# Optimization experiments

Hardware: AMD Instinct MI355X
Metric: run time of the kernel (lower is better)

Reference implementation:

```python
import jax, jax.numpy as jnp
import numpy as np

B, S, D, N = 8, 4096, 1024, 64
SHIFT_FRAC = 0.5
LN_EPS = 1e-5


def setup_inputs() -> dict:
    key = jax.random.key(0)
    ks = jax.random.split(key, 6)
    x = jax.random.normal(ks[0], (B, S, D), jnp.float32)
    # decay in (-1, 0] so w = exp(decay) in (e^-1, 1] -- stable recurrence
    time_decay = -jax.random.uniform(ks[1], (N,), jnp.float32)
    time_first = 0.1 * jax.random.normal(ks[2], (N,), jnp.float32)
    key_w = jax.random.normal(ks[3], (N, D), jnp.float32) / np.float32(np.sqrt(D))
    value_w = jax.random.normal(ks[4], (N, D), jnp.float32) / np.float32(np.sqrt(D))
    output_w = jax.random.normal(ks[5], (D, N), jnp.float32) / np.float32(np.sqrt(N))
    time_shift_gates = jnp.ones((D,), jnp.float32)
    ln_w = jnp.ones((D,), jnp.float32)
    ln_b = jnp.zeros((D,), jnp.float32)
    return dict(x=x, time_decay=time_decay, time_first=time_first,
                key_w=key_w, value_w=value_w, output_w=output_w,
                time_shift_gates=time_shift_gates, ln_w=ln_w, ln_b=ln_b)


def reference(x, time_decay, time_first, key_w, value_w, output_w,
              time_shift_gates, ln_w, ln_b):
    b, s, d = x.shape
    # ---- token shift (blend current token with shifted sequence) ----
    shift = max(1, int(s * SHIFT_FRAC))
    x_cat = jnp.concatenate([x[:, shift:, :], x[:, :-shift, :]], axis=1)  # (b,s,d)
    g = jax.nn.sigmoid(time_shift_gates)
    x_shift = x_cat * g + x * (1.0 - g)
    # ---- LayerNorm (biased variance, eps=1e-5, affine) ----
    mu = jnp.mean(x_shift, axis=-1, keepdims=True)
    var = jnp.mean((x_shift - mu) ** 2, axis=-1, keepdims=True)
    x_norm = (x_shift - mu) * jax.lax.rsqrt(var + LN_EPS) * ln_w + ln_b
    # ---- K/V projections, batched over all timesteps ----
    k = jnp.einsum('bsd,nd->bsn', x_norm, key_w)   # (b,s,N)
    v = jnp.einsum('bsd,nd->bsn', x_norm, value_w)  # (b,s,N)
    w = jnp.exp(time_decay)                          # (N,)
    wkv = jnp.exp(-jnp.exp(time_first) * k) * v      # (b,s,N)
    # ---- sequential linear recurrence: states = states*w + wkv_t ----
    def step(states, wkv_t):
        states = states * w + wkv_t
        return states, states
    init = jnp.zeros((b, wkv.shape[-1]), x.dtype)
    last_states, states_seq = jax.lax.scan(step, init, jnp.swapaxes(wkv, 0, 1))  # (s,b,N)
    # ---- output projection batched outside the loop ----
    output = jnp.einsum('sbn,dn->bsd', states_seq, output_w)  # (b,s,d)
    # dropout is identity in eval mode
    return output, last_states
```

## Files before the change

kernel.cpp:

```cpp
#include <hip/hip_runtime.h>
#include <math.h>

#define B_ 8
#define S_ 4096
#define D_ 1024
#define N_ 64
#define SHIFT_ 2048
#define LCH 32
#define CCH 128
#define MTOT (B_*S_)
#define EPS_ 1e-5f

typedef __attribute__((ext_vector_type(8))) short v8s;
typedef __attribute__((ext_vector_type(4))) float v4f;

static __device__ __forceinline__ short f2bf(float f) {
    unsigned int u = __float_as_uint(f);
    u += 0x7fffu + ((u >> 16) & 1u);
    return (short)(u >> 16);
}

__global__ __launch_bounds__(256) void k_conv(
    const float* __restrict__ keyw, const float* __restrict__ valw,
    const float* __restrict__ ow, const float* __restrict__ tf,
    const float* __restrict__ tsg,
    short* __restrict__ wbf, short* __restrict__ owbf,
    float* __restrict__ etf, float* __restrict__ g) {
    int i = blockIdx.x * 256 + threadIdx.x;
    if (i < 65536)          wbf[i] = f2bf(keyw[i]);
    else if (i < 131072)    wbf[i] = f2bf(valw[i - 65536]);
    else if (i < 196608)    owbf[i - 131072] = f2bf(ow[i - 131072]);
    else if (i < 196672)    etf[i - 196608] = __expf(tf[i - 196608]);
    else if (i < 197696) {
        int j = i - 196672;
        g[j] = 1.0f / (1.0f + __expf(-tsg[j]));
    }
}

__global__ __launch_bounds__(256) void k_stats_fused(
    const float* __restrict__ x, const float* __restrict__ g,
    const float* __restrict__ lnw, const float* __restrict__ lnb,
    short* __restrict__ xn) {
    int b = blockIdx.x >> 11;
    int t = blockIdx.x & 2047;
    const float* rowa = x + ((size_t)(b * S_ + t)) * D_;
    const float* rowb = rowa + (size_t)SHIFT_ * D_;
    int c = threadIdx.x * 4;
    float4 xa = *(const float4*)(rowa + c);
    float4 xb = *(const float4*)(rowb + c);
    float4 gg = *(const float4*)(g + c);
    float av[4] = {xa.x, xa.y, xa.z, xa.w};
    float bv[4] = {xb.x, xb.y, xb.z, xb.w};
    float gv[4] = {gg.x, gg.y, gg.z, gg.w};
    float u[4], w2[4];
    float s1 = 0.f, q1 = 0.f, s2 = 0.f, q2 = 0.f;
#pragma unroll
    for (int j = 0; j < 4; j++) {
        u[j]  = gv[j] * bv[j] + (1.f - gv[j]) * av[j];
        w2[j] = gv[j] * av[j] + (1.f - gv[j]) * bv[j];
        s1 += u[j];  q1 += u[j] * u[j];
        s2 += w2[j]; q2 += w2[j] * w2[j];
    }
    __shared__ float red[4][4];
    int lane = threadIdx.x & 63, wv = threadIdx.x >> 6;
#pragma unroll
    for (int off = 32; off > 0; off >>= 1) {
        s1 += __shfl_down(s1, off);
        q1 += __shfl_down(q1, off);
        s2 += __shfl_down(s2, off);
        q2 += __shfl_down(q2, off);
    }
    if (lane == 0) { red[wv][0] = s1; red[wv][1] = q1; red[wv][2] = s2; red[wv][3] = q2; }
    __syncthreads();
    float S1 = red[0][0] + red[1][0] + red[2][0] + red[3][0];
    float Q1 = red[0][1] + red[1][1] + red[2][1] + red[3][1];
    float S2 = red[0][2] + red[1][2] + red[2][2] + red[3][2];
    float Q2 = red[0][3] + red[1][3] + red[2][3] + red[3][3];
    float m1 = S1 * (1.f / D_), m2 = S2 * (1.f / D_);
    float rs1 = rsqrtf(Q1 * (1.f / D_) - m1 * m1 + EPS_);
    float rs2 = rsqrtf(Q2 * (1.f / D_) - m2 * m2 + EPS_);
    float4 lw = *(const float4*)(lnw + c);
    float4 lb = *(const float4*)(lnb + c);
    float lwv[4] = {lw.x, lw.y, lw.z, lw.w};
    float lbv[4] = {lb.x, lb.y, lb.z, lb.w};
    short o1[4], o2[4];
#pragma unroll
    for (int j = 0; j < 4; j++) {
        o1[j] = f2bf((u[j]  - m1) * rs1 * lwv[j] + lbv[j]);
        o2[j] = f2bf((w2[j] - m2) * rs2 * lwv[j] + lbv[j]);
    }
    short* d1 = xn + ((size_t)(b * S_ + t)) * D_ + c;
    short* d2 = d1 + (size_t)SHIFT_ * D_;
    *(short4*)d1 = make_short4(o1[0], o1[1], o1[2], o1[3]);
    *(short4*)d2 = make_short4(o2[0], o2[1], o2[2], o2[3]);
}

__global__ __launch_bounds__(512) void k_proj_mx(
    const short* __restrict__ xn, const short* __restrict__ wbf,
    const float* __restrict__ etf, const float* __restrict__ tdec,
    float* __restrict__ wkv, float* __restrict__ Acar) {
    __shared__ float C[64 * 132];
    int tid = threadIdx.x, wid = tid >> 6, lane = tid & 63;
    int wm = wid >> 1, wn = wid & 1;
    int quad = lane >> 4, l15 = lane & 15;
    int m0 = blockIdx.x * 64;
    const short* ab = xn + ((size_t)(m0 + wm * 16 + l15)) * D_ + quad * 8;
    const short* bb = wbf + ((size_t)(wn * 64 + l15)) * D_ + quad * 8;
    v4f acc[4];
#pragma unroll
    for (int j = 0; j < 4; j++) acc[j] = (v4f)0.f;

#pragma unroll 4
    for (int k0 = 0; k0 < D_; k0 += 32) {
        v8s a0 = *(const v8s*)(ab + k0);
        v8s b0 = *(const v8s*)(bb + k0);
        v8s b1 = *(const v8s*)(bb + (size_t)16 * D_ + k0);
        v8s b2 = *(const v8s*)(bb + (size_t)32 * D_ + k0);
        v8s b3 = *(const v8s*)(bb + (size_t)48 * D_ + k0);
        acc[0] = __builtin_amdgcn_mfma_f32_16x16x32_bf16(a0, b0, acc[0], 0, 0, 0);
        acc[1] = __builtin_amdgcn_mfma_f32_16x16x32_bf16(a0, b1, acc[1], 0, 0, 0);
        acc[2] = __builtin_amdgcn_mfma_f32_16x16x32_bf16(a0, b2, acc[2], 0, 0, 0);
        acc[3] = __builtin_amdgcn_mfma_f32_16x16x32_bf16(a0, b3, acc[3], 0, 0, 0);
    }
#pragma unroll
    for (int j = 0; j < 4; j++)
#pragma unroll
        for (int r = 0; r < 4; r++)
            C[(wm * 16 + quad * 4 + r) * 132 + wn * 64 + j * 16 + l15] = acc[j][r];
    __syncthreads();

    int tok = tid >> 3, n0 = (tid & 7) * 8;
    float* orow = wkv + ((size_t)(m0 + tok)) * N_ + n0;
    float os[8];
#pragma unroll
    for (int jj = 0; jj < 8; jj++) {
        float kv = C[tok * 132 + n0 + jj];
        float vv = C[tok * 132 + 64 + n0 + jj];
        os[jj] = __expf(-etf[n0 + jj] * kv) * vv;
    }
    *(float4*)(orow + 0) = make_float4(os[0], os[1], os[2], os[3]);
    *(float4*)(orow + 4) = make_float4(os[4], os[5], os[6], os[7]);
#pragma unroll
    for (int jj = 0; jj < 8; jj++) C[tok * 132 + n0 + jj] = os[jj];
    __syncthreads();

    if (tid < 128) {
        int c = tid >> 6, n = tid & 63;
        float w = expf(tdec[n]);
        float s = 0.f;
#pragma unroll
        for (int i = 0; i < LCH; i++) s = s * w + C[(c * 32 + i) * 132 + n];
        Acar[((size_t)blockIdx.x * 2 + c) * N_ + n] = s;
    }
}

__global__ __launch_bounds__(256) void k_stats_mu(const float* __restrict__ x,
                                                  const float* __restrict__ g,
                                                  float* __restrict__ mu,
                                                  float* __restrict__ rstd) {
    int b = blockIdx.x >> 11;
    int t = blockIdx.x & 2047;
    const float* rowa = x + ((size_t)(b * S_ + t)) * D_;
    const float* rowb = rowa + (size_t)SHIFT_ * D_;
    int c = threadIdx.x * 4;
    float4 xa = *(const float4*)(rowa + c);
    float4 xb = *(const float4*)(rowb + c);
    float4 gg = *(const float4*)(g + c);
    float av[4] = {xa.x, xa.y, xa.z, xa.w};
    float bv[4] = {xb.x, xb.y, xb.z, xb.w};
    float gv[4] = {gg.x, gg.y, gg.z, gg.w};
    float s1 = 0.f, q1 = 0.f, s2 = 0.f, q2 = 0.f;
#pragma unroll
    for (int j = 0; j < 4; j++) {
        float u  = gv[j] * bv[j] + (1.f - gv[j]) * av[j];
        float w2 = gv[j] * av[j] + (1.f - gv[j]) * bv[j];
        s1 += u;  q1 += u * u;
        s2 += w2; q2 += w2 * w2;
    }
    __shared__ float red[4][4];
    int lane = threadIdx.x & 63, wv = threadIdx.x >> 6;
#pragma unroll
    for (int off = 32; off > 0; off >>= 1) {
        s1 += __shfl_down(s1, off);
        q1 += __shfl_down(q1, off);
        s2 += __shfl_down(s2, off);
        q2 += __shfl_down(q2, off);
    }
    if (lane == 0) { red[wv][0] = s1; red[wv][1] = q1; red[wv][2] = s2; red[wv][3] = q2; }
    __syncthreads();
    if (threadIdx.x == 0) {
        float S1 = 0, Q1 = 0, S2 = 0, Q2 = 0;
#pragma unroll
        for (int i = 0; i < 4; i++) { S1 += red[i][0]; Q1 += red[i][1]; S2 += red[i][2]; Q2 += red[i][3]; }
        float m1 = S1 * (1.f / D_), m2 = S2 * (1.f / D_);
        float v1 = Q1 * (1.f / D_) - m1 * m1;
        float v2 = Q2 * (1.f / D_) - m2 * m2;
        int m = b * S_ + t;
        mu[m] = m1;           rstd[m] = rsqrtf(v1 + EPS_);
        mu[m + SHIFT_] = m2;  rstd[m + SHIFT_] = rsqrtf(v2 + EPS_);
    }
}

__global__ __launch_bounds__(256) void k_proj_fp32(
    const float* __restrict__ x, const float* __restrict__ keyw,
    const float* __restrict__ valw, const float* __restrict__ g,
    const float* __restrict__ lnw, const float* __restrict__ lnb,
    const float* __restrict__ tf, const float* __restrict__ mu,
    const float* __restrict__ rstd, float* __restrict__ wkv) {
    __shared__ float smem[64 * 132];
    float* As = smem;
    float* Bs = smem + 64 * 36;

    int m0 = blockIdx.x * 64;
    int b = m0 >> 12;
    int t0 = m0 & 4095;
    int t2 = (t0 + SHIFT_) & 4095;
    const float* xa_base = x + ((size_t)(b * S_ + t0)) * D_;
    const float* xb_base = x + ((size_t)(b * S_ + t2)) * D_;

    int tid = threadIdx.x;
    int ty = tid >> 4, tx = tid & 15;
    int tokA = tid >> 3;
    int cA = (tid & 7) * 4;

    float mu0 = mu[m0 + tokA],      rs0 = rstd[m0 + tokA];
    float mu1 = mu[m0 + tokA + 32], rs1 = rstd[m0 + tokA + 32];

    int nB = tid >> 1;
    int halfB = tid & 1;
    const float* wrow = (nB < 64) ? (keyw + (size_t)nB * D_)
                                  : (valw + (size_t)(nB - 64) * D_);

    float acc[4][8];
#pragma unroll
    for (int i = 0; i < 4; i++)
#pragma unroll
        for (int j = 0; j < 8; j++) acc[i][j] = 0.f;

    for (int kk0 = 0; kk0 < D_; kk0 += 32) {
        float4 gg = *(const float4*)(g + kk0 + cA);
        float4 lw = *(const float4*)(lnw + kk0 + cA);
        float4 lb = *(const float4*)(lnb + kk0 + cA);
        float gv[4] = {gg.x, gg.y, gg.z, gg.w};
        float lwv[4] = {lw.x, lw.y, lw.z, lw.w};
        float lbv[4] = {lb.x, lb.y, lb.z, lb.w};
#pragma unroll
        for (int r = 0; r < 2; r++) {
            int tok = tokA + r * 32;
            float4 xa = *(const float4*)(xa_base + (size_t)tok * D_ + kk0 + cA);
            float4 xb = *(const float4*)(xb_base + (size_t)tok * D_ + kk0 + cA);
            float xav[4] = {xa.x, xa.y, xa.z, xa.w};
            float xbv[4] = {xb.x, xb.y, xb.z, xb.w};
            float m_ = r ? mu1 : mu0;
            float rs_ = r ? rs1 : rs0;
#pragma unroll
            for (int j = 0; j < 4; j++) {
                float xs = gv[j] * xbv[j] + (1.f - gv[j]) * xav[j];
                As[tok * 36 + cA + j] = (xs - m_) * rs_ * lwv[j] + lbv[j];
            }
        }
#pragma unroll
        for (int cc = 0; cc < 16; cc += 4) {
            int kk = halfB * 16 + cc;
            float4 wv4 = *(const float4*)(wrow + kk0 + kk);
            Bs[(kk + 0) * 132 + nB] = wv4.x;
            Bs[(kk + 1) * 132 + nB] = wv4.y;
            Bs[(kk + 2) * 132 + nB] = wv4.z;
            Bs[(kk + 3) * 132 + nB] = wv4.w;
        }
        __syncthreads();
#pragma unroll
        for (int kk = 0; kk < 32; kk++) {
            float a0 = As[(ty * 4 + 0) * 36 + kk];
            float a1 = As[(ty * 4 + 1) * 36 + kk];
            float a2 = As[(ty * 4 + 2) * 36 + kk];
            float a3 = As[(ty * 4 + 3) * 36 + kk];
            float bvv[8];
#pragma unroll
            for (int j = 0; j < 8; j++) bvv[j] = Bs[kk * 132 + tx * 8 + j];
#pragma unroll
            for (int j = 0; j < 8; j++) {
                acc[0][j] = fmaf(a0, bvv[j], acc[0][j]);
                acc[1][j] = fmaf(a1, bvv[j], acc[1][j]);
                acc[2][j] = fmaf(a2, bvv[j], acc[2][j]);
                acc[3][j] = fmaf(a3, bvv[j], acc[3][j]);
            }
        }
        __syncthreads();
    }
#pragma unroll
    for (int i = 0; i < 4; i++)
#pragma unroll
        for (int j = 0; j < 8; j++)
            smem[(ty * 4 + i) * 132 + tx * 8 + j] = acc[i][j];
    __syncthreads();
    {
        int tok = tid >> 2;
        int n0 = (tid & 3) * 16;
        float* orow = wkv + ((size_t)(m0 + tok)) * N_ + n0;
#pragma unroll
        for (int jj = 0; jj < 16; jj++) {
            int n = n0 + jj;
            float kv = smem[tok * 132 + n];
            float vv = smem[tok * 132 + 64 + n];
            orow[jj] = __expf(-__expf(tf[n]) * kv) * vv;
        }
    }
}

__global__ __launch_bounds__(64) void k_chunk(const float* __restrict__ wkv,
                                              const float* __restrict__ tdec,
                                              float* __restrict__ Acar) {
    int idx = blockIdx.x;
    int n = threadIdx.x;
    float w = expf(tdec[n]);
    const float* p = wkv + (size_t)idx * (LCH * N_) + n;
    float s = 0.f;
#pragma unroll
    for (int i = 0; i < LCH; i++) s = s * w + p[i * N_];
    Acar[idx * N_ + n] = s;
}

__global__ __launch_bounds__(64) void k_carry(const float* __restrict__ Acar,
                                              const float* __restrict__ tdec,
                                              float* __restrict__ Cin,
                                              float* __restrict__ last) {
    int b = blockIdx.x;
    int n = threadIdx.x;
    float wL = expf(tdec[n] * (float)LCH);
    float c = 0.f;
#pragma unroll 16
    for (int ch = 0; ch < CCH; ch++) {
        Cin[(b * CCH + ch) * N_ + n] = c;
        c = c * wL + Acar[(b * CCH + ch) * N_ + n];
    }
    last[b * N_ + n] = c;
}

__global__ __launch_bounds__(64) void k_rescan(const float* __restrict__ wkv,
                                               const float* __restrict__ Cin,
                                               const float* __restrict__ tdec,
                                               short* __restrict__ st) {
    int idx = blockIdx.x;
    int n = threadIdx.x;
    float w = expf(tdec[n]);
    float s = Cin[idx * N_ + n];
    const float* p = wkv + (size_t)idx * (LCH * N_) + n;
    short* q = st + (size_t)idx * (LCH * N_) + n;
#pragma unroll
    for (int i = 0; i < LCH; i++) { s = s * w + p[i * N_]; q[i * N_] = f2bf(s); }
}

__global__ __launch_bounds__(256) void k_out_mx(const short* __restrict__ st,
                                                const short* __restrict__ owbf,
                                                float* __restrict__ out) {
    __shared__ float C[64 * 132];
    int tid = threadIdx.x, wid = tid >> 6, lane = tid & 63;
    int wm = wid >> 1, wn = wid & 1;
    int quad = lane >> 4, l15 = lane & 15;
    int m0 = (blockIdx.x >> 3) * 64;
    int d0 = (blockIdx.x & 7) * 128;
    const short* ab = st + ((size_t)(m0 + wm * 32 + l15)) * N_ + quad * 8;
    const short* bb = owbf + ((size_t)(d0 + wn * 64 + l15)) * N_ + quad * 8;
    v4f acc[2][4];
#pragma unroll
    for (int i = 0; i < 2; i++)
#pragma unroll
        for (int j = 0; j < 4; j++) acc[i][j] = (v4f)0.f;
#pragma unroll
    for (int ks = 0; ks < 2; ks++) {
        v8s a0 = *(const v8s*)(ab + ks * 32);
        v8s a1 = *(const v8s*)(ab + 16 * N_ + ks * 32);
        v8s b0 = *(const v8s*)(bb + ks * 32);
        v8s b1 = *(const v8s*)(bb + 16 * N_ + ks * 32);
        v8s b2 = *(const v8s*)(bb + 32 * N_ + ks * 32);
        v8s b3 = *(const v8s*)(bb + 48 * N_ + ks * 32);
        acc[0][0] = __builtin_amdgcn_mfma_f32_16x16x32_bf16(a0, b0, acc[0][0], 0, 0, 0);
        acc[0][1] = __builtin_amdgcn_mfma_f32_16x16x32_bf16(a0, b1, acc[0][1], 0, 0, 0);
        acc[0][2] = __builtin_amdgcn_mfma_f32_16x16x32_bf16(a0, b2, acc[0][2], 0, 0, 0);
        acc[0][3] = __builtin_amdgcn_mfma_f32_16x16x32_bf16(a0, b3, acc[0][3], 0, 0, 0);
        acc[1][0] = __builtin_amdgcn_mfma_f32_16x16x32_bf16(a1, b0, acc[1][0], 0, 0, 0);
        acc[1][1] = __builtin_amdgcn_mfma_f32_16x16x32_bf16(a1, b1, acc[1][1], 0, 0, 0);
        acc[1][2] = __builtin_amdgcn_mfma_f32_16x16x32_bf16(a1, b2, acc[1][2], 0, 0, 0);
        acc[1][3] = __builtin_amdgcn_mfma_f32_16x16x32_bf16(a1, b3, acc[1][3], 0, 0, 0);
    }
#pragma unroll
    for (int i = 0; i < 2; i++)
#pragma unroll
        for (int j = 0; j < 4; j++)
#pragma unroll
            for (int r = 0; r < 4; r++)
                C[(wm * 32 + i * 16 + quad * 4 + r) * 132 + wn * 64 + j * 16 + l15] = acc[i][j][r];
    __syncthreads();
    int rrow = tid >> 3;
    int ccol = (tid & 7) * 4;
#pragma unroll
    for (int rep = 0; rep < 2; rep++) {
        int row = rep * 32 + rrow;
        float* orow = out + ((size_t)(m0 + row)) * D_ + d0;
        const float* crow = &C[row * 132];
#pragma unroll
        for (int k = 0; k < 4; k++) {
            int col = ccol + k * 32;
            *(float4*)(orow + col) = *(const float4*)(crow + col);
        }
    }
}

extern "C" void kernel_launch(void* const* d_in, const int* in_sizes, int n_in,
                              void* d_out, int out_size, void* d_ws, size_t ws_size,
                              hipStream_t stream) {
    const float* x    = (const float*)d_in[0];
    const float* tdec = (const float*)d_in[1];
    const float* tf   = (const float*)d_in[2];
    const float* keyw = (const float*)d_in[3];
    const float* valw = (const float*)d_in[4];
    const float* ow   = (const float*)d_in[5];
    const float* tsg  = (const float*)d_in[6];
    const float* lnw  = (const float*)d_in[7];
    const float* lnb  = (const float*)d_in[8];
    float* out = (float*)d_out;
    float* ws  = (float*)d_ws;

    float* g     = ws;
    float* etf   = g + 1024;
    short* wbf   = (short*)(etf + 64);
    short* owbf  = (short*)(ws + 66624);
    float* mu    = ws + 99392;
    float* rstd  = mu + 32768;
    float* wkv   = rstd + 32768;
    float* Acar  = wkv + 2097152;
    float* Cin   = Acar + 65536;
    short* stbf  = (short*)(Cin + 65536);
    short* xnorm = (short*)(ws + 3441728);
    const size_t NEED_PRIMARY = (size_t)(3441728 + 16777216) * 4;

    k_conv<<<773, 256, 0, stream>>>(keyw, valw, ow, tf, tsg, wbf, owbf, etf, g);

    if (ws_size >= NEED_PRIMARY) {
        k_stats_fused<<<B_ * (S_ / 2), 256, 0, stream>>>(x, g, lnw, lnb, xnorm);
        k_proj_mx<<<MTOT / 64, 512, 0, stream>>>(xnorm, wbf, etf, tdec, wkv, Acar);
    } else {
        k_stats_mu<<<B_ * (S_ / 2), 256, 0, stream>>>(x, g, mu, rstd);
        k_proj_fp32<<<MTOT / 64, 256, 0, stream>>>(x, keyw, valw, g, lnw, lnb, tf, mu, rstd, wkv);
        k_chunk <<<B_ * CCH, 64, 0, stream>>>(wkv, tdec, Acar);
    }
    k_carry <<<B_, 64, 0, stream>>>(Acar, tdec, Cin, out + (size_t)MTOT * D_);
    k_rescan<<<B_ * CCH, 64, 0, stream>>>(wkv, Cin, tdec, stbf);
    k_out_mx<<<(MTOT / 64) * 8, 256, 0, stream>>>(stbf, owbf, out);
}
```

Before: 346.2 us.

## Stage projection GEMM tiles in LDS with async double-buffered global loads

The K/V projection kernel now copies A (xnorm) and B (weights) tiles into LDS using direct global-to-LDS loads, with an XOR swizzle and double buffering over 64-wide K steps. Each of 4 waves computes a 32x64 output tile instead of 16x64, and the block size drops from 512 to 256 threads. Previously every wave streamed its operands straight from global memory, so the shared weight tile was refetched per wave. The change adds LDS pressure (48KB per block), which may lower occupancy.

```diff
diff --git a/kernel.cpp b/kernel.cpp
--- a/kernel.cpp
+++ b/kernel.cpp
@@ -18,6 +18,13 @@
     unsigned int u = __float_as_uint(f);
     u += 0x7fffu + ((u >> 16) & 1u);
     return (short)(u >> 16);
+}
+
+static __device__ __forceinline__ void gl_lds16(const void* g, void* l) {
+    __builtin_amdgcn_global_load_lds(
+        (const __attribute__((address_space(1))) unsigned int*)g,
+        (__attribute__((address_space(3))) unsigned int*)l,
+        16, 0, 0);
 }
 
 __global__ __launch_bounds__(256) void k_conv(
@@ -95,53 +102,102 @@
     *(short4*)d2 = make_short4(o2[0], o2[1], o2[2], o2[3]);
 }
 
-__global__ __launch_bounds__(512) void k_proj_mx(
+__global__ __launch_bounds__(256) void k_proj_mx(
     const short* __restrict__ xn, const short* __restrict__ wbf,
     const float* __restrict__ etf, const float* __restrict__ tdec,
     float* __restrict__ wkv, float* __restrict__ Acar) {
-    __shared__ float C[64 * 132];
+    __shared__ __align__(16) char lds[49152];
+    char* Ab = lds;
+    char* Bb = lds + 16384;
+    float* C = (float*)lds;
+
     int tid = threadIdx.x, wid = tid >> 6, lane = tid & 63;
     int wm = wid >> 1, wn = wid & 1;
     int quad = lane >> 4, l15 = lane & 15;
     int m0 = blockIdx.x * 64;
-    const short* ab = xn + ((size_t)(m0 + wm * 16 + l15)) * D_ + quad * 8;
-    const short* bb = wbf + ((size_t)(wn * 64 + l15)) * D_ + quad * 8;
-    v4f acc[4];
-#pragma unroll
-    for (int j = 0; j < 4; j++) acc[j] = (v4f)0.f;
-
-#pragma unroll 4
-    for (int k0 = 0; k0 < D_; k0 += 32) {
-        v8s a0 = *(const v8s*)(ab + k0);
-        v8s b0 = *(const v8s*)(bb + k0);
-        v8s b1 = *(const v8s*)(bb + (size_t)16 * D_ + k0);
-        v8s b2 = *(const v8s*)(bb + (size_t)32 * D_ + k0);
-        v8s b3 = *(const v8s*)(bb + (size_t)48 * D_ + k0);
-        acc[0] = __builtin_amdgcn_mfma_f32_16x16x32_bf16(a0, b0, acc[0], 0, 0, 0);
-        acc[1] = __builtin_amdgcn_mfma_f32_16x16x32_bf16(a0, b1, acc[1], 0, 0, 0);
-        acc[2] = __builtin_amdgcn_mfma_f32_16x16x32_bf16(a0, b2, acc[2], 0, 0, 0);
-        acc[3] = __builtin_amdgcn_mfma_f32_16x16x32_bf16(a0, b3, acc[3], 0, 0, 0);
-    }
-#pragma unroll
-    for (int j = 0; j < 4; j++)
-#pragma unroll
-        for (int r = 0; r < 4; r++)
-            C[(wm * 16 + quad * 4 + r) * 132 + wn * 64 + j * 16 + l15] = acc[j][r];
-    __syncthreads();
-
-    int tok = tid >> 3, n0 = (tid & 7) * 8;
+
+    const char* xb = (const char*)(xn + (size_t)m0 * D_);
+    const char* wb = (const char*)wbf;
+
+    v4f acc[2][4];
+#pragma unroll
+    for (int i = 0; i < 2; i++)
+#pragma unroll
+        for (int j = 0; j < 4; j++) acc[i][j] = (v4f)0.f;
+
+    auto stage = [&](int buf, int k0) {
+#pragma unroll
+        for (int j = 0; j < 2; ++j) {
+            int s = j * 256 + wid * 64 + lane;
+            int r = s >> 3, cu = s & 7;
+            gl_lds16(xb + (size_t)r * 2048 + k0 * 2 + ((cu ^ (r & 7)) << 4),
+                     Ab + buf * 8192 + (j * 256 + wid * 64) * 16);
+        }
+#pragma unroll
+        for (int j = 0; j < 4; ++j) {
+            int s = j * 256 + wid * 64 + lane;
+            int r = s >> 3, cu = s & 7;
+            gl_lds16(wb + (size_t)r * 2048 + k0 * 2 + ((cu ^ (r & 7)) << 4),
+                     Bb + buf * 16384 + (j * 256 + wid * 64) * 16);
+        }
+    };
+    auto ldA = [&](int buf, int r, int cu) -> v8s {
+        return *(const v8s*)(Ab + buf * 8192 + r * 128 + ((cu ^ (r & 7)) << 4));
+    };
+    auto ldB = [&](int buf, int r, int cu) -> v8s {
+        return *(const v8s*)(Bb + buf * 16384 + r * 128 + ((cu ^ (r & 7)) << 4));
+    };
+
+    stage(0, 0);
+    int cur = 0;
+    for (int kt = 0; kt < 16; ++kt) {
+        __syncthreads();
+        if (kt < 15) stage(cur ^ 1, (kt + 1) * 64);
+#pragma unroll
+        for (int kk2 = 0; kk2 < 2; ++kk2) {
+            int cu = kk2 * 4 + quad;
+            v8s a0 = ldA(cur, wm * 32 + l15, cu);
+            v8s a1 = ldA(cur, wm * 32 + 16 + l15, cu);
+            v8s b0 = ldB(cur, wn * 64 + l15, cu);
+            v8s b1 = ldB(cur, wn * 64 + 16 + l15, cu);
+            v8s b2 = ldB(cur, wn * 64 + 32 + l15, cu);
+            v8s b3 = ldB(cur, wn * 64 + 48 + l15, cu);
+            acc[0][0] = __builtin_amdgcn_mfma_f32_16x16x32_bf16(a0, b0, acc[0][0], 0, 0, 0);
+            acc[0][1] = __builtin_amdgcn_mfma_f32_16x16x32_bf16(a0, b1, acc[0][1], 0, 0, 0);
+            acc[0][2] = __builtin_amdgcn_mfma_f32_16x16x32_bf16(a0, b2, acc[0][2], 0, 0, 0);
+            acc[0][3] = __builtin_amdgcn_mfma_f32_16x16x32_bf16(a0, b3, acc[0][3], 0, 0, 0);
+            acc[1][0] = __builtin_amdgcn_mfma_f32_16x16x32_bf16(a1, b0, acc[1][0], 0, 0, 0);
+            acc[1][1] = __builtin_amdgcn_mfma_f32_16x16x32_bf16(a1, b1, acc[1][1], 0, 0, 0);
+            acc[1][2] = __builtin_amdgcn_mfma_f32_16x16x32_bf16(a1, b2, acc[1][2], 0, 0, 0);
+            acc[1][3] = __builtin_amdgcn_mfma_f32_16x16x32_bf16(a1, b3, acc[1][3], 0, 0, 0);
+        }
+        cur ^= 1;
+    }
+    __syncthreads();
+
+#pragma unroll
+    for (int i = 0; i < 2; i++)
+#pragma unroll
+        for (int j = 0; j < 4; j++)
+#pragma unroll
+            for (int r = 0; r < 4; r++)
+                C[(wm * 32 + i * 16 + quad * 4 + r) * 132 + wn * 64 + j * 16 + l15] = acc[i][j][r];
+    __syncthreads();
+
+    int tok = tid >> 2, n0 = (tid & 3) * 16;
     float* orow = wkv + ((size_t)(m0 + tok)) * N_ + n0;
-    float os[8];
-#pragma unroll
-    for (int jj = 0; jj < 8; jj++) {
+    float os[16];
+#pragma unroll
+    for (int jj = 0; jj < 16; jj++) {
         float kv = C[tok * 132 + n0 + jj];
         float vv = C[tok * 132 + 64 + n0 + jj];
         os[jj] = __expf(-etf[n0 + jj] * kv) * vv;
     }
-    *(float4*)(orow + 0) = make_float4(os[0], os[1], os[2], os[3]);
-    *(float4*)(orow + 4) = make_float4(os[4], os[5], os[6], os[7]);
-#pragma unroll
-    for (int jj = 0; jj < 8; jj++) C[tok * 132 + n0 + jj] = os[jj];
+#pragma unroll
+    for (int jj = 0; jj < 16; jj += 4)
+        *(float4*)(orow + jj) = make_float4(os[jj], os[jj + 1], os[jj + 2], os[jj + 3]);
+#pragma unroll
+    for (int jj = 0; jj < 16; jj++) C[tok * 132 + n0 + jj] = os[jj];
     __syncthreads();
 
     if (tid < 128) {
@@ -439,7 +495,7 @@
 
     if (ws_size >= NEED_PRIMARY) {
         k_stats_fused<<<B_ * (S_ / 2), 256, 0, stream>>>(x, g, lnw, lnb, xnorm);
-        k_proj_mx<<<MTOT / 64, 512, 0, stream>>>(xnorm, wbf, etf, tdec, wkv, Acar);
+        k_proj_mx<<<MTOT / 64, 256, 0, stream>>>(xnorm, wbf, etf, tdec, wkv, Acar);
     } else {
         k_stats_mu<<<B_ * (S_ / 2), 256, 0, stream>>>(x, g, mu, rstd);
         k_proj_fp32<<<MTOT / 64, 256, 0, stream>>>(x, keyw, valw, g, lnw, lnb, tf, mu, rstd, wkv);
```

Result: faster. 288.9 us (-16.5%).
